# Kernel optimization log

Hardware: AMD Instinct MI355X
Metric: run time of the kernel (lower is better)

Reference implementation:

```python
import jax, jax.numpy as jnp
import numpy as np

K = 3            # CRF kernel size
THETA0 = 0.5     # color bandwidth
THETA1 = 30.0    # spatial bandwidth
ALPHA0 = 3.0     # kernel scale
BASE = 0.45      # label clamping base
CRF_ITERS = 10   # mean-field iterations
NMS_SIGMA = 2.0  # gaussian matrix-NMS sigma


def _unfold(x, k=K):
    # torch.nn.Unfold(k, stride=1, padding=k//2): (B, C, H, W) -> (B, C, k*k, H*W)
    B, C, H, W = x.shape
    p = k // 2
    xp = jnp.pad(x, ((0, 0), (0, 0), (p, p), (p, p)))
    patches = jnp.stack([xp[:, :, i:i + H, j:j + W]
                         for i in range(k) for j in range(k)], axis=2)
    return patches.reshape(B, C, k * k, H * W)


def _matrix_nms(seg_masks, cate_labels, cate_scores, sigma=NMS_SIGMA):
    n = seg_masks.shape[0]
    m = seg_masks.reshape(n, -1).astype(jnp.float32)
    sum_m = m.sum(axis=1)                         # (n,)
    inter = m @ m.T                               # (n, n)
    union = sum_m[None, :] + sum_m[:, None] - inter
    triu = jnp.triu(jnp.ones((n, n), dtype=bool), k=1)
    iou = jnp.where(triu, inter / union, 0.0)
    label_eq = (cate_labels[None, :] == cate_labels[:, None]) & triu
    decay_iou = jnp.where(label_eq, iou, 0.0)
    comp = decay_iou.max(axis=0)                  # compensate IoU per candidate
    decay = jnp.exp(-sigma * decay_iou ** 2)
    compm = jnp.exp(-sigma * comp ** 2)[:, None]  # broadcast over columns (torch expand+T)
    coef = (decay / compm).min(axis=0)
    return cate_scores * coef


def _crf(feature_map, x, targets):
    B, C, H, W = feature_map.shape
    k2 = K * K
    # gaussian pairwise kernel from (shifted) color features
    fm = feature_map + 10.0
    uf = _unfold(fm)                              # (B, C, k2, H*W)
    idx = np.arange(k2)
    spatial = ((idx // K - K // 2) ** 2 + (idx % K - K // 2) ** 2).astype(np.float32)
    color = -((uf - fm.reshape(B, C, 1, H * W)) ** 2).sum(axis=1) / (2.0 * THETA0 ** 2)
    kernel = ALPHA0 * jnp.exp(color - jnp.asarray(spatial)[None, :, None] / (2.0 * THETA1 ** 2))
    kernel = kernel[:, None]                      # (B, 1, k2, H*W)

    # unary init
    xt = x * targets
    xt = (xt > 0.5).astype(jnp.float32) * (1.0 - 2.0 * BASE) + BASE
    ret = jnp.concatenate([1.0 - xt, xt], axis=1)  # (B, 2, H, W)
    ones_t = jnp.ones_like(targets)
    for _ in range(CRF_ITERS):
        uf_x = _unfold(-jnp.log(ret.reshape(2 * B, 1, H, W))).reshape(B, 2, k2, H * W)
        aggre = (uf_x * kernel).sum(axis=2)        # (B, 2, H*W)
        f = jnp.exp(-aggre).reshape(B, 2, H, W)
        f = f * jnp.concatenate([ones_t, targets], axis=1)  # gate fg channel by targets
        f = f + 1e-6
        f = f / f.sum(axis=1, keepdims=True)
        ret = (f > 0.5).astype(jnp.float32) * (1.0 - 2.0 * BASE) + BASE
    masks = (ret[:, 1:] > 0.5).astype(jnp.float32)  # (B, 1, H, W)
    count = masks.reshape(B, -1).sum(axis=1)
    valid = ((count >= H * W * 0.05) & (count <= H * W * 0.95)).astype(jnp.float32)
    return masks, valid


def setup_inputs() -> dict:
    key = jax.random.key(0)
    k1, k2, k3, k4, k5, k6 = jax.random.split(key, 6)
    n, h, w = 256, 128, 128
    ni, c = 64, 3
    seg_masks = (jax.random.uniform(k1, (n, h, w)) > 0.5).astype(jnp.float32)
    cate_scores = jnp.sort(jax.random.uniform(k2, (n,)))[::-1]
    feature_map = jax.random.uniform(k3, (ni, c, h, w))
    x = jax.random.uniform(k4, (ni, 1, h, w))
    targets = (jax.random.uniform(k5, (ni, 1, h, w)) > 0.3).astype(jnp.float32)
    cate_labels = jax.random.randint(k6, (n,), 0, 80, dtype=jnp.int64)
    return {"seg_masks": seg_masks, "cate_scores": cate_scores,
            "feature_map": feature_map, "x": x, "targets": targets,
            "cate_labels": cate_labels}


def reference(seg_masks, cate_scores, feature_map, x, targets, cate_labels):
    scores = _matrix_nms(seg_masks, cate_labels, cate_scores)
    masks, valid = _crf(feature_map, x, targets)
    return scores, masks, valid
```

## Files before the change

kernel.cpp:

```cpp
#include <hip/hip_runtime.h>
#include <stdint.h>

#define HW 16384
#define NI 64
#define NM 256
#define WORDS 256

#define PR 136
#define WROWS 52
#define PSZ (WROWS * PR)
#define SR 34

#define LDS_PLANE_BYTES (4 * PSZ * 4)
#define LDS_STW_BYTES   (2 * WROWS * SR * 4)
#define LDS_TOTAL       (LDS_PLANE_BYTES + LDS_STW_BYTES + 16)

#define OFF_PACKED (2u << 20)
#define OFF_DIOUT  0x280000u
#define OFF_COMPM  0x2C0000u
#define OFF_CNT    0x2C1000u

__device__ __forceinline__ void build_planes_row(
    const float* __restrict__ fb, float* __restrict__ plane, const int y,
    const int xc, const int wrow, const int q, const bool inimg) {
    #pragma clang fp contract(off)
    float c0[4], c1[4], c2[4];
    if (inimg) {
        const int pp = y * 128 + xc;
        float4 cv0 = *(const float4*)&fb[pp];
        float4 cv1 = *(const float4*)&fb[HW + pp];
        float4 cv2 = *(const float4*)&fb[2 * HW + pp];
        c0[0]=cv0.x+10.0f; c0[1]=cv0.y+10.0f; c0[2]=cv0.z+10.0f; c0[3]=cv0.w+10.0f;
        c1[0]=cv1.x+10.0f; c1[1]=cv1.y+10.0f; c1[2]=cv1.z+10.0f; c1[3]=cv1.w+10.0f;
        c2[0]=cv2.x+10.0f; c2[1]=cv2.y+10.0f; c2[2]=cv2.z+10.0f; c2[3]=cv2.w+10.0f;
    }
    #pragma unroll
    for (int k = 0; k < 4; ++k) {
        const int dy = (k < 3) ? -1 : 0;
        const int dx = (k < 3) ? (k - 1) : -1;
        float res[4] = {0.0f, 0.0f, 0.0f, 0.0f};
        if (inimg) {
            const int ny = y + dy;
            if ((unsigned)ny < 128u) {
                #pragma unroll
                for (int j = 0; j < 4; ++j) {
                    const int nx = xc + j + dx;
                    if ((unsigned)nx < 128u) {
                        const int qq = ny * 128 + nx;
                        float u0 = fb[qq] + 10.0f;
                        float u1 = fb[HW + qq] + 10.0f;
                        float u2 = fb[2 * HW + qq] + 10.0f;
                        float d0 = u0 - c0[j], d1 = u1 - c1[j], d2 = u2 - c2[j];
                        float ss = d0 * d0;
                        ss = ss + d1 * d1;
                        ss = ss + d2 * d2;
                        float color = (-ss) / 0.5f;
                        float sp = (float)(dy * dy + dx * dx) / 1800.0f;
                        res[j] = 3.0f * expf(color - sp);
                    }
                }
            }
        }
        *(float4*)&plane[k * PSZ + wrow * PR + 4 + xc] =
            make_float4(res[0], res[1], res[2], res[3]);
        if (q == 0)
            *(float4*)&plane[k * PSZ + wrow * PR + 0] = make_float4(0, 0, 0, 0);
        if (q == 31)
            *(float4*)&plane[k * PSZ + wrow * PR + 132] = make_float4(0, 0, 0, 0);
    }
}

__device__ __forceinline__ void stage_init_row(
    const float* __restrict__ x, const float* __restrict__ targets,
    uint32_t* __restrict__ stw0, uint32_t* __restrict__ stw1, const int img,
    const int y, const int wrow, const int q, const int xc, const bool inimg) {
    #pragma clang fp contract(off)
    uint32_t st = 0;
    if (inimg) {
        const size_t gp = (size_t)img * HW + y * 128 + xc;
        const float4 xv = *(const float4*)(x + gp);
        const float4 tv = *(const float4*)(targets + gp);
        float xs[4] = {xv.x, xv.y, xv.z, xv.w};
        float ts[4] = {tv.x, tv.y, tv.z, tv.w};
        #pragma unroll
        for (int j = 0; j < 4; ++j) {
            float xt = xs[j] * ts[j];
            int b1 = (xt > 0.5f) ? 1 : 0;
            int tb = (ts[j] > 0.5f) ? 1 : 0;
            st |= (uint32_t)(b1 | ((b1 ^ 1) << 1) | (tb << 2)) << (8 * j);
        }
    }
    stw0[wrow * SR + 1 + q] = st;
    if (!inimg) stw1[wrow * SR + 1 + q] = 0;
    if (q == 0)  { stw0[wrow * SR + 0]  = 0; stw1[wrow * SR + 0]  = 0; }
    if (q == 31) { stw0[wrow * SR + 33] = 0; stw1[wrow * SR + 33] = 0; }
}

__device__ __forceinline__ uint32_t crf_cell(
    const float* __restrict__ plane, const uint32_t* __restrict__ sw,
    const int rbase, const int sbase, uint32_t (&pin)[9], uint32_t& powv,
    bool& haveprev, uint32_t& wcen_out) {
    #pragma clang fp contract(off)
    const float l45 = 0.7985076962177716f;
    const float l55 = 0.5978370007556204f;
    uint32_t in9[9];
    #pragma unroll
    for (int r = 0; r < 3; ++r) {
        const int base = sbase + (r - 1) * SR;
        in9[r * 3 + 0] = sw[base - 1];
        in9[r * 3 + 1] = sw[base];
        in9[r * 3 + 2] = sw[base + 1];
    }
    const uint32_t wcen = in9[4];
    wcen_out = wcen;
    bool same = haveprev;
    #pragma unroll
    for (int m = 0; m < 9; ++m) same = same && (in9[m] == pin[m]);
    if (same) return powv;

    float lx1r[3][6], lx0r[3][6];
    #pragma unroll
    for (int r = 0; r < 3; ++r) {
        const uint32_t wm = in9[r * 3 + 0];
        const uint32_t wc = in9[r * 3 + 1];
        const uint32_t wp = in9[r * 3 + 2];
        unsigned char b[6];
        b[0] = wm >> 24;
        b[1] = wc & 0xff; b[2] = (wc >> 8) & 0xff;
        b[3] = (wc >> 16) & 0xff; b[4] = wc >> 24;
        b[5] = wp & 0xff;
        #pragma unroll
        for (int m = 0; m < 6; ++m) {
            lx1r[r][m] = (b[m] & 1) ? l55 : l45;
            lx0r[r][m] = (b[m] & 2) ? l55 : l45;
        }
    }
    float4 p0a = *(const float4*)&plane[0 * PSZ + rbase];
    float4 p1a = *(const float4*)&plane[1 * PSZ + rbase];
    float4 p2a = *(const float4*)&plane[2 * PSZ + rbase];
    float4 p3a = *(const float4*)&plane[3 * PSZ + rbase];
    float4 p0b = *(const float4*)&plane[0 * PSZ + rbase + PR];
    float4 p1b = *(const float4*)&plane[1 * PSZ + rbase + PR];
    float4 p2b = *(const float4*)&plane[2 * PSZ + rbase + PR];
    float s5 = plane[3 * PSZ + rbase + 4];
    float s6 = plane[2 * PSZ + rbase + PR - 1];
    float s8 = plane[0 * PSZ + rbase + PR + 4];
    const float kw[9][4] = {
        {p0a.x, p0a.y, p0a.z, p0a.w},
        {p1a.x, p1a.y, p1a.z, p1a.w},
        {p2a.x, p2a.y, p2a.z, p2a.w},
        {p3a.x, p3a.y, p3a.z, p3a.w},
        {3.0f, 3.0f, 3.0f, 3.0f},
        {p3a.y, p3a.z, p3a.w, s5},
        {s6, p2b.x, p2b.y, p2b.z},
        {p1b.x, p1b.y, p1b.z, p1b.w},
        {p0b.y, p0b.z, p0b.w, s8}};
    float a0[4] = {0.f, 0.f, 0.f, 0.f}, a1[4] = {0.f, 0.f, 0.f, 0.f};
    #pragma unroll
    for (int k = 0; k < 9; ++k) {
        const int r = k / 3, m0 = k % 3;
        #pragma unroll
        for (int j = 0; j < 4; ++j) {
            const float kwv = kw[k][j];
            const float t1 = lx1r[r][j + m0] * kwv;
            const float t0 = lx0r[r][j + m0] * kwv;
            a1[j] = a1[j] + t1;
            a0[j] = a0[j] + t0;
        }
    }
    uint32_t ow = 0;
    #pragma unroll
    for (int j = 0; j < 4; ++j) {
        const unsigned char sc = (wcen >> (8 * j)) & 0xffu;
        const float tval = (sc & 4) ? 1.0f : 0.0f;
        const float e1 = expf(-a1[j]);
        const float e0 = expf(-a0[j]);
        const float m1 = e1 * tval;
        const float f1 = m1 + 1e-6f;
        const float f0 = e0 + 1e-6f;
        const float den = f0 + f1;
        const float r1 = f1 / den;
        const float r0v = f0 / den;
        const int s1 = (r1 > 0.5f) ? 1 : 0;
        const int s0 = (r0v > 0.5f) ? 1 : 0;
        ow |= (uint32_t)(s1 | (s0 << 1) | (sc & 4)) << (8 * j);
    }
    #pragma unroll
    for (int m = 0; m < 9; ++m) pin[m] = in9[m];
    powv = ow;
    haveprev = true;
    return ow;
}

__global__ __launch_bounds__(832, 4) void crf10_kernel(
    const float* __restrict__ feat, const float* __restrict__ seg,
    unsigned long long* __restrict__ packed, const float* __restrict__ x,
    const float* __restrict__ targets, float* __restrict__ out,
    int* __restrict__ counters) {
    #pragma clang fp contract(off)
    extern __shared__ char smem[];
    float* plane = (float*)smem;
    uint32_t* stw0 = (uint32_t*)(smem + LDS_PLANE_BYTES);
    uint32_t* stw1 = stw0 + WROWS * SR;
    int* chg = (int*)(smem + LDS_PLANE_BYTES + LDS_STW_BYTES);
    uint32_t* const stwb[2] = {stw0, stw1};

    const int tid = threadIdx.x, bid = blockIdx.x;
    const int img = bid >> 2;
    const int r0 = (bid & 3) * 32;
    const int relp = tid >> 5;
    const int q = tid & 31;
    const int xc = q * 4;
    const int wrowA = 2 * relp, wrowB = 2 * relp + 1;
    const int yA = r0 - 10 + wrowA, yB = yA + 1;
    const bool inA = (unsigned)yA < 128u, inB = (unsigned)yB < 128u;
    const int rbaseA = wrowA * PR + 4 + xc, rbaseB = wrowB * PR + 4 + xc;
    const int sbaseA = wrowA * SR + 1 + q,  sbaseB = wrowB * SR + 1 + q;
    const float* fb = feat + (size_t)img * 3 * HW;

    {
        const int wave = tid >> 6, lane = tid & 63;
        const int gw = bid * 13 + wave;
        for (int gwi = gw; gwi < 65536; gwi += 3328) {
            const int i = gwi >> 8, w = gwi & 255;
            float v = seg[(size_t)i * HW + w * 64 + lane];
            unsigned long long m = __ballot(v > 0.5f);
            if (lane == 0) packed[w * NM + i] = m;
        }
    }

    build_planes_row(fb, plane, yA, xc, wrowA, q, inA);
    build_planes_row(fb, plane, yB, xc, wrowB, q, inB);
    stage_init_row(x, targets, stw0, stw1, img, yA, wrowA, q, xc, inA);
    stage_init_row(x, targets, stw0, stw1, img, yB, wrowB, q, xc, inB);
    __syncthreads();

    uint32_t pinA[9], pinB[9];
    uint32_t powvA = 0, powvB = 0;
    bool hpA = false, hpB = false;
    int cur = 0;
    for (int s = 0; s < 10; ++s) {
        if (tid == 0) *chg = 0;
        __syncthreads();
        const int lo = (r0 - 9 + s < 0) ? 0 : r0 - 9 + s;
        const int hi = (r0 + 41 - s > 128) ? 128 : r0 + 41 - s;
        const uint32_t* sw = stwb[cur];
        uint32_t* swn = stwb[cur ^ 1];
        bool changed = false;
        if (yA >= lo && yA < hi) {
            uint32_t wcen;
            uint32_t ow = crf_cell(plane, sw, rbaseA, sbaseA, pinA, powvA, hpA, wcen);
            swn[sbaseA] = ow;
            changed = (ow != wcen);
        }
        if (yB >= lo && yB < hi) {
            uint32_t wcen;
            uint32_t ow = crf_cell(plane, sw, rbaseB, sbaseB, pinB, powvB, hpB, wcen);
            swn[sbaseB] = ow;
            changed = changed || (ow != wcen);
        }
        unsigned long long bal = __ballot(changed);
        if ((tid & 63) == 0 && bal) atomicOr(chg, 1);
        __syncthreads();
        if (*chg == 0) break;
        cur ^= 1;
    }

    int cnt = 0;
    {
        const uint32_t* swf = stwb[cur];
        float* om = out + NM + (size_t)img * HW;
        if (yA >= r0 && yA < r0 + 32) {
            const uint32_t w = swf[sbaseA];
            *(float4*)(om + yA * 128 + xc) =
                make_float4((float)(w & 1), (float)((w >> 8) & 1),
                            (float)((w >> 16) & 1), (float)((w >> 24) & 1));
            cnt += __popc(w & 0x01010101u);
        }
        if (yB >= r0 && yB < r0 + 32) {
            const uint32_t w = swf[sbaseB];
            *(float4*)(om + yB * 128 + xc) =
                make_float4((float)(w & 1), (float)((w >> 8) & 1),
                            (float)((w >> 16) & 1), (float)((w >> 24) & 1));
            cnt += __popc(w & 0x01010101u);
        }
    }
    __syncthreads();
    {
        int* cred = (int*)plane;
        cred[tid] = cnt;
        if (tid < 192) cred[832 + tid] = 0;
        __syncthreads();
        for (int off = 512; off > 0; off >>= 1) {
            if (tid < off) cred[tid] += cred[tid + off];
            __syncthreads();
        }
        if (tid == 0) counters[bid] = cred[0];
    }
}

__global__ __launch_bounds__(256) void diou_compm_kernel(
    const unsigned long long* __restrict__ packed, const int* __restrict__ labels,
    float* __restrict__ diouT, float* __restrict__ compm) {
    #pragma clang fp contract(off)
    __shared__ unsigned long long colj[WORDS];
    __shared__ float red[NM];
    const int j = blockIdx.x, i = threadIdx.x;
    colj[i] = packed[i * NM + j];
    __syncthreads();
    int inter = 0, si = 0, sj = 0;
    for (int w = 0; w < WORDS; ++w) {
        unsigned long long a = colj[w];
        unsigned long long b = packed[w * NM + i];
        inter += __popcll(a & b);
        sj += __popcll(a);
        si += __popcll(b);
    }
    float d = 0.0f;
    if (j > i && labels[i] == labels[j]) {
        float u = (float)(si + sj - inter);
        d = (float)inter / u;
    }
    diouT[j * NM + i] = d;
    red[i] = d;
    __syncthreads();
    for (int off = 128; off > 0; off >>= 1) {
        if (i < off) red[i] = fmaxf(red[i], red[i + off]);
        __syncthreads();
    }
    if (i == 0) {
        float m = red[0];
        float t = m * m;
        compm[j] = expf(-2.0f * t);
    }
}

__global__ __launch_bounds__(256) void coef_valid_kernel(
    const float* __restrict__ scores, const float* __restrict__ diouT,
    const float* __restrict__ compm, const int* __restrict__ counters,
    float* __restrict__ out) {
    #pragma clang fp contract(off)
    __shared__ float red[NM];
    const int bid = blockIdx.x, tid = threadIdx.x;
    float d = diouT[bid * NM + tid];
    float dd = d * d;
    float dec = expf(-2.0f * dd);
    red[tid] = dec / compm[tid];
    __syncthreads();
    for (int off = 128; off > 0; off >>= 1) {
        if (tid < off) red[tid] = fminf(red[tid], red[tid + off]);
        __syncthreads();
    }
    if (tid == 0) out[bid] = scores[bid] * red[0];
    if (bid == 0 && tid < NI) {
        int c = counters[4 * tid] + counters[4 * tid + 1] +
                counters[4 * tid + 2] + counters[4 * tid + 3];
        out[NM + (size_t)NI * HW + tid] = (c >= 820 && c <= 15564) ? 1.0f : 0.0f;
    }
}

extern "C" void kernel_launch(void* const* d_in, const int* in_sizes, int n_in,
                              void* d_out, int out_size, void* d_ws, size_t ws_size,
                              hipStream_t stream) {
    const float* seg = (const float*)d_in[0];
    const float* cate_scores = (const float*)d_in[1];
    const float* feat = (const float*)d_in[2];
    const float* x = (const float*)d_in[3];
    const float* targets = (const float*)d_in[4];
    const int* labels = (const int*)d_in[5];
    float* out = (float*)d_out;
    char* ws = (char*)d_ws;

    unsigned long long* packed = (unsigned long long*)(ws + OFF_PACKED);
    float* diouT = (float*)(ws + OFF_DIOUT);
    float* compm = (float*)(ws + OFF_COMPM);
    int* counters = (int*)(ws + OFF_CNT);

    static bool attr_done = false;
    if (!attr_done) {
        (void)hipFuncSetAttribute((const void*)crf10_kernel,
                                  hipFuncAttributeMaxDynamicSharedMemorySize,
                                  LDS_TOTAL);
        attr_done = true;
    }

    crf10_kernel<<<256, 832, LDS_TOTAL, stream>>>(feat, seg, packed, x, targets,
                                                  out, counters);
    diou_compm_kernel<<<NM, 256, 0, stream>>>(packed, labels, diouT, compm);
    coef_valid_kernel<<<NM, 256, 0, stream>>>(cate_scores, diouT, compm,
                                              counters, out);
}
```

Baseline: 170.4 us.

## Share neighbor rows between paired cells, hoist plane loads, drop per-iteration barrier

Each thread's two vertically adjacent cells (rows A and B) now share their overlapping state-word loads. The kernel-weight plane values for row A, and the parts reused by row B, are loaded into registers once before the mean-field loop instead of on every iteration. The per-iteration reset barrier is removed by keeping a separate change flag for each iteration in LDS, initialized before the loop. This saves LDS traffic and one __syncthreads per iteration, at the cost of more live registers under an 832-thread launch bound, which could cause spills.

```diff
diff --git a/kernel.cpp b/kernel.cpp
--- a/kernel.cpp
+++ b/kernel.cpp
@@ -13,7 +13,7 @@
 
 #define LDS_PLANE_BYTES (4 * PSZ * 4)
 #define LDS_STW_BYTES   (2 * WROWS * SR * 4)
-#define LDS_TOTAL       (LDS_PLANE_BYTES + LDS_STW_BYTES + 16)
+#define LDS_TOTAL       (LDS_PLANE_BYTES + LDS_STW_BYTES + 64)
 
 #define OFF_PACKED (2u << 20)
 #define OFF_DIOUT  0x280000u
@@ -96,28 +96,12 @@
     if (q == 31) { stw0[wrow * SR + 33] = 0; stw1[wrow * SR + 33] = 0; }
 }
 
-__device__ __forceinline__ uint32_t crf_cell(
-    const float* __restrict__ plane, const uint32_t* __restrict__ sw,
-    const int rbase, const int sbase, uint32_t (&pin)[9], uint32_t& powv,
-    bool& haveprev, uint32_t& wcen_out) {
+__device__ __forceinline__ uint32_t crf_core(const float (&kw)[9][4],
+                                             const uint32_t (&in9)[9]) {
     #pragma clang fp contract(off)
     const float l45 = 0.7985076962177716f;
     const float l55 = 0.5978370007556204f;
-    uint32_t in9[9];
-    #pragma unroll
-    for (int r = 0; r < 3; ++r) {
-        const int base = sbase + (r - 1) * SR;
-        in9[r * 3 + 0] = sw[base - 1];
-        in9[r * 3 + 1] = sw[base];
-        in9[r * 3 + 2] = sw[base + 1];
-    }
     const uint32_t wcen = in9[4];
-    wcen_out = wcen;
-    bool same = haveprev;
-    #pragma unroll
-    for (int m = 0; m < 9; ++m) same = same && (in9[m] == pin[m]);
-    if (same) return powv;
-
     float lx1r[3][6], lx0r[3][6];
     #pragma unroll
     for (int r = 0; r < 3; ++r) {
@@ -135,26 +119,6 @@
             lx0r[r][m] = (b[m] & 2) ? l55 : l45;
         }
     }
-    float4 p0a = *(const float4*)&plane[0 * PSZ + rbase];
-    float4 p1a = *(const float4*)&plane[1 * PSZ + rbase];
-    float4 p2a = *(const float4*)&plane[2 * PSZ + rbase];
-    float4 p3a = *(const float4*)&plane[3 * PSZ + rbase];
-    float4 p0b = *(const float4*)&plane[0 * PSZ + rbase + PR];
-    float4 p1b = *(const float4*)&plane[1 * PSZ + rbase + PR];
-    float4 p2b = *(const float4*)&plane[2 * PSZ + rbase + PR];
-    float s5 = plane[3 * PSZ + rbase + 4];
-    float s6 = plane[2 * PSZ + rbase + PR - 1];
-    float s8 = plane[0 * PSZ + rbase + PR + 4];
-    const float kw[9][4] = {
-        {p0a.x, p0a.y, p0a.z, p0a.w},
-        {p1a.x, p1a.y, p1a.z, p1a.w},
-        {p2a.x, p2a.y, p2a.z, p2a.w},
-        {p3a.x, p3a.y, p3a.z, p3a.w},
-        {3.0f, 3.0f, 3.0f, 3.0f},
-        {p3a.y, p3a.z, p3a.w, s5},
-        {s6, p2b.x, p2b.y, p2b.z},
-        {p1b.x, p1b.y, p1b.z, p1b.w},
-        {p0b.y, p0b.z, p0b.w, s8}};
     float a0[4] = {0.f, 0.f, 0.f, 0.f}, a1[4] = {0.f, 0.f, 0.f, 0.f};
     #pragma unroll
     for (int k = 0; k < 9; ++k) {
@@ -185,10 +149,6 @@
         const int s0 = (r0v > 0.5f) ? 1 : 0;
         ow |= (uint32_t)(s1 | (s0 << 1) | (sc & 4)) << (8 * j);
     }
-    #pragma unroll
-    for (int m = 0; m < 9; ++m) pin[m] = in9[m];
-    powv = ow;
-    haveprev = true;
     return ow;
 }
 
@@ -233,36 +193,107 @@
     build_planes_row(fb, plane, yB, xc, wrowB, q, inB);
     stage_init_row(x, targets, stw0, stw1, img, yA, wrowA, q, xc, inA);
     stage_init_row(x, targets, stw0, stw1, img, yB, wrowB, q, xc, inB);
+    if (tid < 10) chg[tid] = 0;
     __syncthreads();
+
+    const float4 a_p0 = *(const float4*)&plane[0 * PSZ + rbaseA];
+    const float4 a_p1 = *(const float4*)&plane[1 * PSZ + rbaseA];
+    const float4 a_p2 = *(const float4*)&plane[2 * PSZ + rbaseA];
+    const float4 a_p3 = *(const float4*)&plane[3 * PSZ + rbaseA];
+    const float  a_s5 = plane[3 * PSZ + rbaseA + 4];
+    const float4 b_p0 = *(const float4*)&plane[0 * PSZ + rbaseB];
+    const float4 b_p1 = *(const float4*)&plane[1 * PSZ + rbaseB];
+    const float4 b_p2 = *(const float4*)&plane[2 * PSZ + rbaseB];
+    const float4 b_p3 = *(const float4*)&plane[3 * PSZ + rbaseB];
+    const float  b_s5 = plane[3 * PSZ + rbaseB + 4];
+    const float  b_s6 = plane[2 * PSZ + rbaseB - 1];
+    const float  b_s8 = plane[0 * PSZ + rbaseB + 4];
+    const float kwA[9][4] = {
+        {a_p0.x, a_p0.y, a_p0.z, a_p0.w},
+        {a_p1.x, a_p1.y, a_p1.z, a_p1.w},
+        {a_p2.x, a_p2.y, a_p2.z, a_p2.w},
+        {a_p3.x, a_p3.y, a_p3.z, a_p3.w},
+        {3.0f, 3.0f, 3.0f, 3.0f},
+        {a_p3.y, a_p3.z, a_p3.w, a_s5},
+        {b_s6, b_p2.x, b_p2.y, b_p2.z},
+        {b_p1.x, b_p1.y, b_p1.z, b_p1.w},
+        {b_p0.y, b_p0.z, b_p0.w, b_s8}};
 
     uint32_t pinA[9], pinB[9];
     uint32_t powvA = 0, powvB = 0;
     bool hpA = false, hpB = false;
     int cur = 0;
     for (int s = 0; s < 10; ++s) {
-        if (tid == 0) *chg = 0;
-        __syncthreads();
         const int lo = (r0 - 9 + s < 0) ? 0 : r0 - 9 + s;
         const int hi = (r0 + 41 - s > 128) ? 128 : r0 + 41 - s;
+        const bool actA = (yA >= lo) && (yA < hi);
+        const bool actB = (yB >= lo) && (yB < hi);
         const uint32_t* sw = stwb[cur];
         uint32_t* swn = stwb[cur ^ 1];
         bool changed = false;
-        if (yA >= lo && yA < hi) {
-            uint32_t wcen;
-            uint32_t ow = crf_cell(plane, sw, rbaseA, sbaseA, pinA, powvA, hpA, wcen);
-            swn[sbaseA] = ow;
-            changed = (ow != wcen);
-        }
-        if (yB >= lo && yB < hi) {
-            uint32_t wcen;
-            uint32_t ow = crf_cell(plane, sw, rbaseB, sbaseB, pinB, powvB, hpB, wcen);
-            swn[sbaseB] = ow;
-            changed = changed || (ow != wcen);
+        if (actA || actB) {
+            const uint32_t ra0 = sw[sbaseA - 1], ra1 = sw[sbaseA], ra2 = sw[sbaseA + 1];
+            const uint32_t rb0 = sw[sbaseB - 1], rb1 = sw[sbaseB], rb2 = sw[sbaseB + 1];
+            if (actA) {
+                const uint32_t in9[9] = {sw[sbaseA - SR - 1], sw[sbaseA - SR],
+                                         sw[sbaseA - SR + 1], ra0, ra1, ra2,
+                                         rb0, rb1, rb2};
+                bool same = hpA;
+                #pragma unroll
+                for (int m = 0; m < 9; ++m) same = same && (in9[m] == pinA[m]);
+                uint32_t ow;
+                if (same) {
+                    ow = powvA;
+                } else {
+                    ow = crf_core(kwA, in9);
+                    #pragma unroll
+                    for (int m = 0; m < 9; ++m) pinA[m] = in9[m];
+                    powvA = ow;
+                    hpA = true;
+                }
+                swn[sbaseA] = ow;
+                changed = (ow != ra1);
+            }
+            if (actB) {
+                const uint32_t in9[9] = {ra0, ra1, ra2, rb0, rb1, rb2,
+                                         sw[sbaseB + SR - 1], sw[sbaseB + SR],
+                                         sw[sbaseB + SR + 1]};
+                bool same = hpB;
+                #pragma unroll
+                for (int m = 0; m < 9; ++m) same = same && (in9[m] == pinB[m]);
+                uint32_t ow;
+                if (same) {
+                    ow = powvB;
+                } else {
+                    const float4 c_p0 = *(const float4*)&plane[0 * PSZ + rbaseB + PR];
+                    const float4 c_p1 = *(const float4*)&plane[1 * PSZ + rbaseB + PR];
+                    const float4 c_p2 = *(const float4*)&plane[2 * PSZ + rbaseB + PR];
+                    const float  c_s6 = plane[2 * PSZ + rbaseB + PR - 1];
+                    const float  c_s8 = plane[0 * PSZ + rbaseB + PR + 4];
+                    const float kwB[9][4] = {
+                        {b_p0.x, b_p0.y, b_p0.z, b_p0.w},
+                        {b_p1.x, b_p1.y, b_p1.z, b_p1.w},
+                        {b_p2.x, b_p2.y, b_p2.z, b_p2.w},
+                        {b_p3.x, b_p3.y, b_p3.z, b_p3.w},
+                        {3.0f, 3.0f, 3.0f, 3.0f},
+                        {b_p3.y, b_p3.z, b_p3.w, b_s5},
+                        {c_s6, c_p2.x, c_p2.y, c_p2.z},
+                        {c_p1.x, c_p1.y, c_p1.z, c_p1.w},
+                        {c_p0.y, c_p0.z, c_p0.w, c_s8}};
+                    ow = crf_core(kwB, in9);
+                    #pragma unroll
+                    for (int m = 0; m < 9; ++m) pinB[m] = in9[m];
+                    powvB = ow;
+                    hpB = true;
+                }
+                swn[sbaseB] = ow;
+                changed = changed || (ow != rb1);
+            }
         }
         unsigned long long bal = __ballot(changed);
-        if ((tid & 63) == 0 && bal) atomicOr(chg, 1);
+        if ((tid & 63) == 0 && bal) atomicOr(&chg[s], 1);
         __syncthreads();
-        if (*chg == 0) break;
+        if (chg[s] == 0) break;
         cur ^= 1;
     }
 
```

Measured after the change: 167.3 us. No clear change (-1.8%).
